# Performance work log

Measured on AMD Instinct MI355X. Metric: run time of the kernel, lower is better.

## Reference

```python
import jax, jax.numpy as jnp
import numpy as np

# Module-level globals from the original repo
THRES = 1.0           # mempot_thres
DECAY = 1             # decay
DECAY_MULT = (2.0 ** DECAY - 1.0) / (2.0 ** DECAY)  # (m*2^d - m)/2^d == m*DECAY_MULT

NEURONS = (16384, 4096, 4096, 1024)
TSTEPS = 64


def _init_w(key, n_in, n_out):
    return jax.random.normal(key, (n_in, n_out), dtype=jnp.float32) * np.float32(np.sqrt(2.0 / n_in))


def setup_inputs() -> dict:
    key = jax.random.key(0)
    k_img, k1, k2, k3 = jax.random.split(key, 4)
    image = jax.random.uniform(k_img, (128, 128), dtype=jnp.float32)  # flattens to NEURONS[0]
    w1 = _init_w(k1, NEURONS[0], NEURONS[1])
    w2 = _init_w(k2, NEURONS[1], NEURONS[2])
    w3 = _init_w(k3, NEURONS[2], NEURONS[3])
    return {"image": image, "w1": w1, "w2": w2, "w3": w3}


def _lin_step(mempot, spikes_in, w):
    # integrate: sum of weights from firing presynaptic neurons (spike-gated GEMV)
    mempot = mempot + spikes_in.astype(w.dtype) @ w
    fire = mempot >= THRES
    # fire -> subtract threshold; else -> leak decay
    mempot = jnp.where(fire, mempot - THRES, mempot * DECAY_MULT)
    return mempot, fire


def reference(image, w1, w2, w3):
    img = image.reshape(-1)  # nn.Flatten(0, -1)
    n0, n1 = w1.shape
    n2, n3 = w2.shape[1], w3.shape[1]

    def step(carry, _):
        m0, m1, m2, m3, s1_prev, s2_prev = carry
        # input layer: integrate image, fire, NO decay
        m0 = m0 + img
        s0 = m0 >= THRES
        m0 = jnp.where(s0, m0 - THRES, m0)
        # lin1 consumes this timestep's input spikes
        m1, s1 = _lin_step(m1, s0, w1)
        # lin2/lin3 consume the PREVIOUS timestep's spikes (pipeline delay in original)
        m2, s2 = _lin_step(m2, s1_prev, w2)
        m3, s3 = _lin_step(m3, s2_prev, w3)
        return (m0, m1, m2, m3, s1, s2), (s0, s1, s2, s3)

    init = (
        jnp.zeros(n0, jnp.float32), jnp.zeros(n1, jnp.float32),
        jnp.zeros(n2, jnp.float32), jnp.zeros(n3, jnp.float32),
        jnp.zeros(n1, bool), jnp.zeros(n2, bool),
    )
    _, (s0, s1, s2, s3) = jax.lax.scan(step, init, None, length=TSTEPS)

    # original stores spikes[0][tstep] and spikes[k>=1][tstep+1] in (TSTEPS+1)-row buffers
    def pad_tail(s):  # rows 0..T-1 filled, row T zero
        return jnp.concatenate([s, jnp.zeros((1, s.shape[1]), s.dtype)], 0).astype(jnp.float32)

    def pad_head(s):  # row 0 zero, rows 1..T filled
        return jnp.concatenate([jnp.zeros((1, s.shape[1]), s.dtype), s], 0).astype(jnp.float32)

    return (pad_tail(s0), pad_head(s1), pad_head(s2), pad_head(s3))
```

## Files before the change

### kernel.cpp

```cpp
#include <hip/hip_runtime.h>
#include <cstdint>

typedef float f4 __attribute__((ext_vector_type(4)));
typedef short bf8 __attribute__((ext_vector_type(8)));
typedef unsigned int u32;
typedef unsigned int u32x4 __attribute__((ext_vector_type(4)));
typedef unsigned short u16;


__device__ __forceinline__ float uf(u32 x) { return __builtin_bit_cast(float, x); }
__device__ __forceinline__ u32 fu(float x) { return __builtin_bit_cast(u32, x); }

struct FragMap { int amode, bmode, rw[4], cl[4]; };

__device__ __forceinline__ FragMap probe_map()
{
    int l = threadIdx.x & 63;
    u32 lb = fu((float)l) >> 16;
    u32 lbb = lb | (lb << 16);
    u32x4 lv4 = {lbb, lbb, lbb, lbb};
    u32x4 on4 = {0x3F803F80u, 0x3F803F80u, 0x3F803F80u, 0x3F803F80u};
    bf8 lv = __builtin_bit_cast(bf8, lv4);
    bf8 on = __builtin_bit_cast(bf8, on4);
    f4 z = {0.f, 0.f, 0.f, 0.f};
    f4 d1 = __builtin_amdgcn_mfma_f32_16x16x32_bf16(on, lv, z, 0, 0, 0);
    f4 d2 = __builtin_amdgcn_mfma_f32_16x16x32_bf16(lv, on, z, 0, 0, 0);
    FragMap fm; fm.amode = 0; fm.bmode = 0;
#pragma unroll
    for (int r = 0; r < 4; ++r) {
        int v1 = (int)(d1[r] + 0.5f);
        if (v1 >= 768 && v1 <= 1248 && ((v1 - 768) & 31) == 0) { fm.cl[r] = (v1 - 768) >> 5; fm.bmode = 0; }
        else                                                   { fm.cl[r] = (v1 - 48) >> 7;  fm.bmode = 1; }
        int v2 = (int)(d2[r] + 0.5f);
        if (v2 >= 768 && v2 <= 1248 && ((v2 - 768) & 31) == 0) { fm.rw[r] = (v2 - 768) >> 5; fm.amode = 0; }
        else                                                   { fm.rw[r] = (v2 - 48) >> 7;  fm.amode = 1; }
    }
    return fm;
}

__global__ __launch_bounds__(256) void k_input(const float* __restrict__ img,
                                               float* __restrict__ out0,
                                               u16* __restrict__ SA0, int n)
{
    FragMap fm = probe_map();
    int i = blockIdx.x * 256 + threadIdx.x;
    if (i >= n) return;
    int g = (i & 31) >> 3, e = i & 7;
    int lanes[16];
#pragma unroll
    for (int m = 0; m < 16; ++m) lanes[m] = (fm.amode == 0) ? (g * 16 + m) : (m * 4 + g);
    u16* base = SA0 + ((size_t)(i >> 5)) * 2048 + e;
    double m = 0.0;
    double x = (double)img[i];
#pragma unroll
    for (int t = 0; t < 64; ++t) {
        m += x;
        bool fire = (m >= 1.0);
        if (fire) m -= 1.0;
        out0[(size_t)t * n + i] = fire ? 1.0f : 0.0f;
        base[((t >> 4) << 9) + (lanes[t & 15] << 3)] = fire ? (u16)0x3F80 : (u16)0;
    }
    out0[(size_t)64 * n + i] = 0.0f;
}

#define SPLIT2(we, wo, hD, mD, lD) do {                                        \
    u32 he = (we) & 0xFFFF0000u; float r1e = uf(we) - uf(he);                  \
    u32 me = fu(r1e) & 0xFFFF0000u; float r2e = r1e - uf(me); u32 le = fu(r2e);\
    u32 ho = (wo) & 0xFFFF0000u; float r1o = uf(wo) - uf(ho);                  \
    u32 mo = fu(r1o) & 0xFFFF0000u; float r2o = r1o - uf(mo); u32 lo2 = fu(r2o);\
    hD = (he >> 16) | ho; mD = (me >> 16) | mo;                                \
    lD = (le >> 16) | (lo2 & 0xFFFF0000u);                                     \
} while (0)

template<int NOUT>
__global__ __launch_bounds__(64, 2) void k_gemm(const float* __restrict__ W,
                                                const u16* __restrict__ SA,
                                                double* __restrict__ P,
                                                int n_in, int ipc)
{
    FragMap fm = probe_map();
    const int lane = threadIdx.x;
    const int j0   = blockIdx.x * 32;
    const int c    = blockIdx.y;
    const int gB   = (fm.bmode == 0) ? (lane >> 4) : (lane & 3);
    const int nB   = (fm.bmode == 0) ? (lane & 15) : (lane >> 2);

    int i0 = c * ipc;
    int i1 = i0 + ipc; if (i1 > n_in) i1 = n_in;
    int nsteps = (i1 > i0) ? ((i1 - i0) >> 5) : 0;

    double accd[2][4][4];
#pragma unroll
    for (int jt = 0; jt < 2; ++jt)
#pragma unroll
        for (int tt = 0; tt < 4; ++tt)
#pragma unroll
            for (int r = 0; r < 4; ++r) accd[jt][tt][r] = 0.0;

    const size_t wstep = (size_t)32 * NOUT;
    struct Set { const u32* wp; const u16* ap; u32 w[16]; u32x4 a[4]; };
    Set S0_, S1_;
    S0_.wp = (const u32*)W + (size_t)(i0 + gB * 8) * NOUT + j0 + nB;
    S1_.wp = S0_.wp + wstep;
    S0_.ap = SA + (size_t)(i0 >> 5) * 2048 + lane * 8;
    S1_.ap = S0_.ap + 2048;

#define LOADSET(S, sidx) do {                                                  \
        if ((sidx) < nsteps) {                                                 \
            _Pragma("unroll") for (int k = 0; k < 8; ++k) {                    \
                S.w[k]     = S.wp[(size_t)k * NOUT];                           \
                S.w[8 + k] = S.wp[(size_t)k * NOUT + 16];                      \
            }                                                                  \
            _Pragma("unroll") for (int tt = 0; tt < 4; ++tt)                   \
                S.a[tt] = *(const u32x4*)(S.ap + tt * 512);                    \
        } else {                                                               \
            _Pragma("unroll") for (int k = 0; k < 16; ++k) S.w[k] = 0;         \
            _Pragma("unroll") for (int tt = 0; tt < 4; ++tt)                   \
                S.a[tt] = (u32x4){0, 0, 0, 0};                                 \
        }                                                                      \
        S.wp += 2 * wstep; S.ap += 4096;                                       \
    } while (0)

#define COMPUTESET(S) do {                                                     \
        _Pragma("unroll") for (int jt = 0; jt < 2; ++jt) {                     \
            u32 hd[4], md[4], ld[4];                                           \
            _Pragma("unroll") for (int p = 0; p < 4; ++p)                      \
                SPLIT2(S.w[jt * 8 + 2 * p], S.w[jt * 8 + 2 * p + 1],           \
                       hd[p], md[p], ld[p]);                                   \
            u32x4 hv = {hd[0], hd[1], hd[2], hd[3]};                           \
            u32x4 mv = {md[0], md[1], md[2], md[3]};                           \
            u32x4 lv = {ld[0], ld[1], ld[2], ld[3]};                           \
            bf8 Bh = __builtin_bit_cast(bf8, hv);                              \
            bf8 Bm = __builtin_bit_cast(bf8, mv);                              \
            bf8 Bl = __builtin_bit_cast(bf8, lv);                              \
            f4 zz = {0.f, 0.f, 0.f, 0.f};                                      \
            _Pragma("unroll") for (int tt = 0; tt < 4; ++tt) {                 \
                bf8 Af = __builtin_bit_cast(bf8, S.a[tt]);                     \
                f4 acc = __builtin_amdgcn_mfma_f32_16x16x32_bf16(Af, Bh, zz, 0, 0, 0); \
                acc = __builtin_amdgcn_mfma_f32_16x16x32_bf16(Af, Bm, acc, 0, 0, 0);   \
                acc = __builtin_amdgcn_mfma_f32_16x16x32_bf16(Af, Bl, acc, 0, 0, 0);   \
                _Pragma("unroll") for (int r = 0; r < 4; ++r)                  \
                    accd[jt][tt][r] += (double)acc[r];                         \
            }                                                                  \
        }                                                                      \
    } while (0)

    LOADSET(S0_, 0);
    LOADSET(S1_, 1);

    int rounds = (nsteps + 1) / 2;
    int s = 0;
    for (int r = 0; r < rounds; ++r) {
        COMPUTESET(S0_); LOADSET(S0_, s + 2);
        COMPUTESET(S1_); LOADSET(S1_, s + 3);
        s += 2;
    }
#undef LOADSET
#undef COMPUTESET

    double* pc = P + (size_t)c * 64 * NOUT;
#pragma unroll
    for (int jt = 0; jt < 2; ++jt)
#pragma unroll
        for (int tt = 0; tt < 4; ++tt)
#pragma unroll
            for (int r = 0; r < 4; ++r)
                pc[(size_t)(tt * 16 + fm.rw[r]) * NOUT + (j0 + jt * 16 + fm.cl[r])] = accd[jt][tt][r];
}

__global__ __launch_bounds__(256) void k_reduceU(const double* __restrict__ P,
                                                 double* __restrict__ U,
                                                 int nchunks, int n_out)
{
    int gid = blockIdx.x * 256 + threadIdx.x;
    int total = 64 * n_out;
    if (gid >= total) return;
    int t = gid / n_out;
    int j = gid - t * n_out;
    double s = 0.0;
    for (int c = 0; c < nchunks; ++c)
        s += P[((size_t)c * 64 + t) * n_out + j];
    U[gid] = s;
}

__global__ __launch_bounds__(256) void k_scan(const double* __restrict__ U,
                                              float* __restrict__ outS,
                                              u16* __restrict__ SAn,
                                              int n_out, int shift)
{
    FragMap fm = probe_map();
    int j = blockIdx.x * 256 + threadIdx.x;
    if (j >= n_out) return;
    int g = (j & 31) >> 3, e = j & 7;
    int lanes[16];
#pragma unroll
    for (int m = 0; m < 16; ++m) lanes[m] = (fm.amode == 0) ? (g * 16 + m) : (m * 4 + g);
    u16* base = SAn ? (SAn + ((size_t)(j >> 5)) * 2048 + e) : (u16*)nullptr;
    double m = 0.0;
    outS[j] = 0.0f;
#pragma unroll
    for (int t = 0; t < 64; ++t) {
        int s = t - shift;
        double u = (s >= 0) ? U[(size_t)s * n_out + j] : 0.0;
        m += u;
        bool fire = (m >= 1.0);
        m = fire ? (m - 1.0) : (m * 0.5);
        outS[(size_t)(t + 1) * n_out + j] = fire ? 1.0f : 0.0f;
        if (base) base[((t >> 4) << 9) + (lanes[t & 15] << 3)] = fire ? (u16)0x3F80 : (u16)0;
    }
}

extern "C" void kernel_launch(void* const* d_in, const int* in_sizes, int n_in_cnt,
                              void* d_out, int out_size, void* d_ws, size_t ws_size,
                              hipStream_t stream)
{
    const float* img = (const float*)d_in[0];
    const float* w1  = (const float*)d_in[1];
    const float* w2  = (const float*)d_in[2];
    const float* w3  = (const float*)d_in[3];

    const int N0 = 16384, N1 = 4096, N2 = 4096, N3 = 1024;

    float* out0 = (float*)d_out;
    float* out1 = out0 + (size_t)65 * N0;
    float* out2 = out1 + (size_t)65 * N1;
    float* out3 = out2 + (size_t)65 * N2;

    char* ws = (char*)d_ws;
    const size_t MB = 1024 * 1024;
    u16*    SA0 = (u16*)(ws);
    u16*    SA1 = (u16*)(ws + 2 * MB);
    u16*    SA2 = (u16*)(ws + 2 * MB + 512 * 1024);
    double* U   = (double*)(ws + 3 * MB);
    double* P   = (double*)(ws + 5 * MB);

    size_t fixed = 5 * MB;
    size_t pbudget = (ws_size > fixed) ? (ws_size - fixed) : 0;

    auto clampi = [](long v, int lo, int hi) { int x = (int)v; if (x < lo) x = lo; if (x > hi) x = hi; return x; };
    int C1 = clampi((long)(pbudget / (512ull * N1)), 1, 24);
    int C2 = clampi((long)(pbudget / (512ull * N2)), 1, 16);
    int C3 = clampi((long)(pbudget / (512ull * N3)), 1, 32);

    auto ipc32 = [](int n_in, int C) { return (((n_in + C - 1) / C) + 31) & ~31; };

    k_input<<<N0 / 256, 256, 0, stream>>>(img, out0, SA0, N0);

    k_gemm<4096><<<dim3(N1 / 32, C1), 64, 0, stream>>>(w1, SA0, P, N0, ipc32(N0, C1));
    k_reduceU<<<(64 * N1) / 256, 256, 0, stream>>>(P, U, C1, N1);
    k_scan<<<N1 / 256, 256, 0, stream>>>(U, out1, SA1, N1, 0);

    k_gemm<4096><<<dim3(N2 / 32, C2), 64, 0, stream>>>(w2, SA1, P, N1, ipc32(N1, C2));
    k_reduceU<<<(64 * N2) / 256, 256, 0, stream>>>(P, U, C2, N2);
    k_scan<<<N2 / 256, 256, 0, stream>>>(U, out2, SA2, N2, 1);

    k_gemm<1024><<<dim3(N3 / 32, C3), 64, 0, stream>>>(w3, SA2, P, N2, ipc32(N2, C3));
    k_reduceU<<<(64 * N3) / 256, 256, 0, stream>>>(P, U, C3, N3);
    k_scan<<<N3 / 256, 256, 0, stream>>>(U, out3, (u16*)nullptr, N3, 1);
}
```

Before: 203.3 us.

## Reduce split-K partials across four waves per block via LDS before global write

Each GEMM block now holds four waves, and each wave handles its own K-chunk. The four double-precision partials are summed in shared memory through a two-level tree with barriers, and only wave 0 writes the combined partial to global memory. This cuts global partial traffic and the number of chunks the reduce kernel has to sum by a factor of four, while keeping the same total K-split. The cost is LDS use, three block barriers, and a change of launch bounds from (64,2) to (256,3), which may alter register allocation and occupancy.

```diff
diff --git a/kernel.cpp b/kernel.cpp
--- a/kernel.cpp
+++ b/kernel.cpp
@@ -73,15 +73,16 @@
 } while (0)
 
 template<int NOUT>
-__global__ __launch_bounds__(64, 2) void k_gemm(const float* __restrict__ W,
-                                                const u16* __restrict__ SA,
-                                                double* __restrict__ P,
-                                                int n_in, int ipc)
+__global__ __launch_bounds__(256, 3) void k_gemm(const float* __restrict__ W,
+                                                 const u16* __restrict__ SA,
+                                                 double* __restrict__ P,
+                                                 int n_in, int ipc)
 {
     FragMap fm = probe_map();
-    const int lane = threadIdx.x;
+    const int lane = threadIdx.x & 63;
+    const int wv   = threadIdx.x >> 6;
     const int j0   = blockIdx.x * 32;
-    const int c    = blockIdx.y;
+    const int c    = blockIdx.y * 4 + wv;
     const int gB   = (fm.bmode == 0) ? (lane >> 4) : (lane & 3);
     const int nB   = (fm.bmode == 0) ? (lane & 15) : (lane >> 2);
 
@@ -158,14 +159,49 @@
 #undef LOADSET
 #undef COMPUTESET
 
-    double* pc = P + (size_t)c * 64 * NOUT;
-#pragma unroll
-    for (int jt = 0; jt < 2; ++jt)
-#pragma unroll
-        for (int tt = 0; tt < 4; ++tt)
-#pragma unroll
-            for (int r = 0; r < 4; ++r)
-                pc[(size_t)(tt * 16 + fm.rw[r]) * NOUT + (j0 + jt * 16 + fm.cl[r])] = accd[jt][tt][r];
+    __shared__ double lds[2][32][64];
+    if (wv >= 2) {
+#pragma unroll
+        for (int jt = 0; jt < 2; ++jt)
+#pragma unroll
+            for (int tt = 0; tt < 4; ++tt)
+#pragma unroll
+                for (int r = 0; r < 4; ++r)
+                    lds[wv - 2][jt * 16 + tt * 4 + r][lane] = accd[jt][tt][r];
+    }
+    __syncthreads();
+    if (wv < 2) {
+#pragma unroll
+        for (int jt = 0; jt < 2; ++jt)
+#pragma unroll
+            for (int tt = 0; tt < 4; ++tt)
+#pragma unroll
+                for (int r = 0; r < 4; ++r)
+                    accd[jt][tt][r] += lds[wv][jt * 16 + tt * 4 + r][lane];
+    }
+    __syncthreads();
+    if (wv == 1) {
+#pragma unroll
+        for (int jt = 0; jt < 2; ++jt)
+#pragma unroll
+            for (int tt = 0; tt < 4; ++tt)
+#pragma unroll
+                for (int r = 0; r < 4; ++r)
+                    lds[0][jt * 16 + tt * 4 + r][lane] = accd[jt][tt][r];
+    }
+    __syncthreads();
+    if (wv == 0) {
+        double* pc = P + (size_t)blockIdx.y * 64 * NOUT;
+#pragma unroll
+        for (int jt = 0; jt < 2; ++jt)
+#pragma unroll
+            for (int tt = 0; tt < 4; ++tt)
+#pragma unroll
+                for (int r = 0; r < 4; ++r) {
+                    double v = accd[jt][tt][r] + lds[0][jt * 16 + tt * 4 + r][lane];
+                    pc[(size_t)(tt * 16 + fm.rw[r]) * NOUT + (j0 + jt * 16 + fm.cl[r])] = v;
+                }
+    }
 }
 
 __global__ __launch_bounds__(256) void k_reduceU(const double* __restrict__ P,
@@ -238,23 +274,24 @@
     size_t pbudget = (ws_size > fixed) ? (ws_size - fixed) : 0;
 
     auto clampi = [](long v, int lo, int hi) { int x = (int)v; if (x < lo) x = lo; if (x > hi) x = hi; return x; };
-    int C1 = clampi((long)(pbudget / (512ull * N1)), 1, 24);
-    int C2 = clampi((long)(pbudget / (512ull * N2)), 1, 16);
-    int C3 = clampi((long)(pbudget / (512ull * N3)), 1, 32);
+    int CB1 = clampi((long)(pbudget / (512ull * N1)), 1, 6);
+    int CB2 = clampi((long)(pbudget / (512ull * N2)), 1, 4);
+    int CB3 = clampi((long)(pbudget / (512ull * N3)), 1, 8);
+    int C1 = CB1 * 4, C2 = CB2 * 4, C3 = CB3 * 4;
 
     auto ipc32 = [](int n_in, int C) { return (((n_in + C - 1) / C) + 31) & ~31; };
 
     k_input<<<N0 / 256, 256, 0, stream>>>(img, out0, SA0, N0);
 
-    k_gemm<4096><<<dim3(N1 / 32, C1), 64, 0, stream>>>(w1, SA0, P, N0, ipc32(N0, C1));
-    k_reduceU<<<(64 * N1) / 256, 256, 0, stream>>>(P, U, C1, N1);
+    k_gemm<4096><<<dim3(N1 / 32, CB1), 256, 0, stream>>>(w1, SA0, P, N0, ipc32(N0, C1));
+    k_reduceU<<<(64 * N1) / 256, 256, 0, stream>>>(P, U, CB1, N1);
     k_scan<<<N1 / 256, 256, 0, stream>>>(U, out1, SA1, N1, 0);
 
-    k_gemm<4096><<<dim3(N2 / 32, C2), 64, 0, stream>>>(w2, SA1, P, N1, ipc32(N1, C2));
-    k_reduceU<<<(64 * N2) / 256, 256, 0, stream>>>(P, U, C2, N2);
+    k_gemm<4096><<<dim3(N2 / 32, CB2), 256, 0, stream>>>(w2, SA1, P, N1, ipc32(N1, C2));
+    k_reduceU<<<(64 * N2) / 256, 256, 0, stream>>>(P, U, CB2, N2);
     k_scan<<<N2 / 256, 256, 0, stream>>>(U, out2, SA2, N2, 1);
 
-    k_gemm<1024><<<dim3(N3 / 32, C3), 64, 0, stream>>>(w3, SA2, P, N2, ipc32(N2, C3));
-    k_reduceU<<<(64 * N3) / 256, 256, 0, stream>>>(P, U, C3, N3);
+    k_gemm<1024><<<dim3(N3 / 32, CB3), 256, 0, stream>>>(w3, SA2, P, N2, ipc32(N2, C3));
+    k_reduceU<<<(64 * N3) / 256, 256, 0, stream>>>(P, U, CB3, N3);
     k_scan<<<N3 / 256, 256, 0, stream>>>(U, out3, (u16*)nullptr, N3, 1);
 }
```

New measurement: 348.6 us. 71.4% more time.
